# Kernel optimization log

Measured on AMD Instinct MI355X. Metric: run time of the kernel, lower is better.

Reference implementation:

```python
import jax, jax.numpy as jnp
import numpy as np

VOCAB = 32000
D = 512
OUT = 1000
L = 2
H = 8
HD = D // H
MAX_SEQ = 128
ALPHA = 0.5
B, S = 8, 128


def _layernorm(h, g, b, eps=1e-5):
    mu = jnp.mean(h, axis=-1, keepdims=True)
    var = jnp.mean(jnp.square(h - mu), axis=-1, keepdims=True)
    return (h - mu) * jax.lax.rsqrt(var + eps) * g + b


def setup_inputs() -> dict:
    key = jax.random.key(0)
    ks = jax.random.split(key, 20)
    sd = 1.0 / np.sqrt(D)
    inp = {
        "x": jax.random.randint(ks[0], (B, S), 0, VOCAB),
        "steps": 20,
        "tok_emb": jax.random.normal(ks[1], (VOCAB, D), jnp.float32) * 0.02,
        "pos_emb": jax.random.normal(ks[2], (MAX_SEQ, D), jnp.float32) * 0.02,
        # per-layer stacked weights (linear as x @ W + b)
        "Wq": jax.random.normal(ks[3], (L, D, D), jnp.float32) * sd,
        "bq": jnp.zeros((L, D), jnp.float32),
        "Wk": jax.random.normal(ks[4], (L, D, D), jnp.float32) * sd,
        "bk": jnp.zeros((L, D), jnp.float32),
        "Wv": jax.random.normal(ks[5], (L, D, D), jnp.float32) * sd,
        "bv": jnp.zeros((L, D), jnp.float32),
        "Wo": jax.random.normal(ks[6], (L, D, D), jnp.float32) * sd,
        "bo": jnp.zeros((L, D), jnp.float32),
        "W1": jax.random.normal(ks[7], (L, D, 2 * D), jnp.float32) * sd,
        "b1": jnp.zeros((L, 2 * D), jnp.float32),
        "W2": jax.random.normal(ks[8], (L, 2 * D, D), jnp.float32) * (1.0 / np.sqrt(2 * D)),
        "b2": jnp.zeros((L, D), jnp.float32),
        "ln1_g": jnp.ones((L, D), jnp.float32),
        "ln1_b": jnp.zeros((L, D), jnp.float32),
        "ln2_g": jnp.ones((L, D), jnp.float32),
        "ln2_b": jnp.zeros((L, D), jnp.float32),
        "head_w": jax.random.normal(ks[9], (D, OUT), jnp.float32) * sd,
        "head_b": jnp.zeros((OUT,), jnp.float32),
    }
    return inp


def _forward(x, steps, tok_emb, pos_emb, Wq, bq, Wk, bk, Wv, bv, Wo, bo,
             W1, b1, W2, b2, ln1_g, ln1_b, ln2_g, ln2_b, head_w, head_b):
    b, s = x.shape
    x_emb = tok_emb[x] + pos_emb[jnp.arange(s)][None, :, :]  # [B,S,D]
    scale = 1.0 / np.sqrt(HD)

    def step(h, _):
        for i in range(L):
            hn = _layernorm(h, ln1_g[i], ln1_b[i])
            q = (hn @ Wq[i] + bq[i]).reshape(b, s, H, HD)
            k = (hn @ Wk[i] + bk[i]).reshape(b, s, H, HD)
            v = (hn @ Wv[i] + bv[i]).reshape(b, s, H, HD)
            scores = jnp.einsum('bqhd,bkhd->bhqk', q, k) * scale
            attn = jax.nn.softmax(scores, axis=-1)
            o = jnp.einsum('bhqk,bkhd->bqhd', attn, v).reshape(b, s, D)
            h = h + (o @ Wo[i] + bo[i])
            hn2 = _layernorm(h, ln2_g[i], ln2_b[i])
            ffn = jax.nn.relu(hn2 @ W1[i] + b1[i]) @ W2[i] + b2[i]
            h_target = h + ffn + x_emb
            h = h + ALPHA * (jnp.tanh(h_target) - h)  # lerp(h, tanh(t), alpha)
        return h, None

    h0 = jnp.zeros_like(x_emb)
    h, _ = jax.lax.scan(step, h0, None, length=steps)
    return h.mean(axis=1) @ head_w + head_b  # [B, OUT]


def reference(x, steps, tok_emb, pos_emb, Wq, bq, Wk, bk, Wv, bv, Wo, bo,
              W1, b1, W2, b2, ln1_g, ln1_b, ln2_g, ln2_b, head_w, head_b):
    return _forward(x, steps, tok_emb, pos_emb, Wq, bq, Wk, bk, Wv, bv, Wo, bo,
                    W1, b1, W2, b2, ln1_g, ln1_b, ln2_g, ln2_b, head_w, head_b)
```

## Files before the change

kernel.cpp:

```cpp
#include <hip/hip_runtime.h>
#include <hip/hip_bf16.h>
#include <math.h>

#define NTOK 1024
#define DM   512
#define NB   256

typedef unsigned short u16;
typedef __attribute__((ext_vector_type(8))) short short8;
typedef __attribute__((ext_vector_type(4))) float f32x4;
typedef __attribute__((ext_vector_type(2))) float f32x2;
typedef __attribute__((address_space(1))) const void* as1cv;
typedef __attribute__((address_space(3))) void* as3v;

#define VM16 0x4F70
#define VM8  0x0F78
#define VM6  0x0F76
#define VM0  0x0F70

__device__ inline u16 f2bf(float f) {
  __hip_bfloat16 h = __float2bfloat16(f);
  return *reinterpret_cast<u16*>(&h);
}
__device__ inline float bf2f(u16 b) {
  union { unsigned u; float f; } x; x.u = (unsigned)b << 16; return x.f;
}
__device__ inline void split8(const float* v, short8& hi, short8& lo) {
#pragma unroll
  for (int j = 0; j < 8; j++) {
    u16 h = f2bf(v[j]);
    hi[j] = (short)h;
    lo[j] = (short)f2bf(v[j] - bf2f(h));
  }
}
__device__ __forceinline__ f32x4 MFMA(short8 a, short8 b, f32x4 c) {
  return __builtin_amdgcn_mfma_f32_16x16x32_bf16(a, b, c, 0, 0, 0);
}
__device__ __forceinline__ void atomAddF(float* p, float v) {
  __hip_atomic_fetch_add(p, v, __ATOMIC_RELAXED, __HIP_MEMORY_SCOPE_AGENT);
}

__device__ __forceinline__ f32x2 ldg_cs2(const float* p) {
  f32x2 r;
  asm volatile("global_load_dwordx2 %0, %1, off sc0 sc1" : "=v"(r) : "v"(p) : "memory");
  return r;
}
__device__ __forceinline__ void vmwait0() {
  asm volatile("s_waitcnt vmcnt(0)" ::: "memory");
  __builtin_amdgcn_sched_barrier(0);
}

enum { EP_RESID = 1, EP_TANHLERP = 3 };

struct KArgs {
  const int* x;
  const float* tok; const float* pos;
  const float* W[6];
  const float* bias6[6];
  const float* ln1g; const float* ln1b; const float* ln2g; const float* ln2b;
  const float* hw; const float* hb;
  float* out;
  float* xe; float* h;
  u16* obh; u16* obl;
  u16* ffh; u16* ffl;
  u16* vT;
  u16* Kg;
  float* hm;
  u16* WTh[6]; u16* WTl[6];
  float* ln1sum; float* ln2sum;
  unsigned* bar;
};

#define SMEM_BYTES 49152

__device__ __forceinline__ void bar_arrive(unsigned* ctr, int tid) {
  __syncthreads();
  if (tid == 0)
    __hip_atomic_fetch_add(ctr, 1u, __ATOMIC_RELEASE, __HIP_MEMORY_SCOPE_AGENT);
}
__device__ __forceinline__ void bar_wait(unsigned* ctr, unsigned target, int tid) {
  if (tid == 0) {
    while (__hip_atomic_load(ctr, __ATOMIC_RELAXED, __HIP_MEMORY_SCOPE_AGENT) < target)
      __builtin_amdgcn_s_sleep(2);
    __builtin_amdgcn_fence(__ATOMIC_ACQUIRE, "agent");
  }
  __syncthreads();
}
__device__ __forceinline__ void bar_arrive_fast(unsigned* myslot, unsigned ph, int tid) {
  asm volatile("s_waitcnt vmcnt(0) lgkmcnt(0)" ::: "memory");
  __syncthreads();
  if (tid == 0)
    __hip_atomic_store(myslot, ph, __ATOMIC_RELAXED, __HIP_MEMORY_SCOPE_AGENT);
}
__device__ __forceinline__ void bar_wait_fast(unsigned* slotbase, unsigned ph, int tid) {
  if (tid < 32) {
    while (__hip_atomic_load(slotbase + tid * 16, __ATOMIC_RELAXED,
                             __HIP_MEMORY_SCOPE_AGENT) < ph)
      __builtin_amdgcn_s_sleep(1);
  }
  __syncthreads();
  asm volatile("buffer_inv sc0" ::: "memory");
  asm volatile("s_waitcnt vmcnt(0)" ::: "memory");
}
__global__ void bar_init(unsigned* bar) {
  for (int i = threadIdx.x; i < 8192; i += 256) bar[i] = 0u;
}

__device__ __forceinline__ void dmaW64(const u16* gbase, int K, int k0, u16* lds, int tid) {
  const int wave = tid >> 6, lane = tid & 63;
#pragma unroll
  for (int i = 0; i < 2; i++) {
    const int lc = wave * 128 + i * 64 + lane;
    const int n = lc >> 3, sl = lc & 7;
    const int c = sl ^ (n & 7);
    const u16* g = gbase + (size_t)n * K + k0 + c * 8;
    u16* dst = lds + (size_t)(wave * 128 + i * 64) * 8;
    __builtin_amdgcn_global_load_lds((as1cv)(const void*)g, (as3v)(void*)dst, 16, 0, 0);
  }
}
__device__ __forceinline__ int boff64(int n, int cp) { return n * 64 + ((cp ^ (n & 7)) << 3); }

__device__ __forceinline__ void dmaW32(const u16* gbase, int K, int k0, u16* lds, int tid) {
  const int wave = tid >> 6, lane = tid & 63;
  const int lc = wave * 64 + lane;
  const int p = lc >> 3, s3 = lc & 7;
  const int c3 = s3 ^ (p & 7);
  const int n = p * 2 + (c3 >> 2);
  const int c = c3 & 3;
  const u16* g = gbase + (size_t)n * K + k0 + c * 8;
  u16* dst = lds + (size_t)(wave * 64) * 8;
  __builtin_amdgcn_global_load_lds((as1cv)(const void*)g, (as3v)(void*)dst, 16, 0, 0);
}
__device__ __forceinline__ int boff32(int n, int cq) {
  const int c3 = ((n & 1) << 2) | cq;
  return ((n >> 1) << 6) + ((c3 ^ ((n >> 1) & 7)) << 3);
}

__device__ __forceinline__ void pfBD2(const u16* bh0, const u16* bl0, int K, char* sm, int tid) {
  dmaW64(bh0, K, 0,  (u16*)sm, tid);
  dmaW64(bl0, K, 0,  (u16*)sm + 4096, tid);
  dmaW64(bh0, K, 64, (u16*)(sm + 16384), tid);
  dmaW64(bl0, K, 64, (u16*)(sm + 16384) + 4096, tid);
}
__device__ __forceinline__ void pfA(const KArgs& a, int l, int head, char* sm, int tid) {
  const size_t o = (size_t)l * 512 * 512 + (size_t)head * 64 * 512;
  const u16* wz[6] = { a.WTh[0] + o, a.WTl[0] + o, a.WTh[1] + o,
                       a.WTl[1] + o, a.WTh[2] + o, a.WTl[2] + o };
#pragma unroll
  for (int z = 0; z < 6; z++) dmaW32(wz[z], 512, 0, (u16*)sm + z * 2048, tid);
}

__device__ void phaseA1(const KArgs& a, int l, int head, int rbk, int grp,
                        const float* ln1, const float* hR,
                        u16* Kg_gh, u16* vT_gh, char* sm, int tid)
{
  const int wave = tid >> 6, lane = tid & 63;
  const int q = lane >> 4, r16 = lane & 15;
  const int wm = (wave >> 1) * 16, wn = (wave & 1) * 32;
  const int R0 = rbk * 32;
  const size_t wOff = (size_t)l * 512 * 512;
  const size_t hOff = (size_t)head * 64 * 512;

  const float* lg = a.ln1g + l * 512;
  const float* lb = a.ln1b + l * 512;
  const u16* wz[6] = { a.WTh[0] + wOff + hOff, a.WTl[0] + wOff + hOff,
                       a.WTh[1] + wOff + hOff, a.WTl[1] + wOff + hOff,
                       a.WTh[2] + wOff + hOff, a.WTl[2] + wOff + hOff };
  u16* buf[2] = { (u16*)sm, (u16*)sm + 12288 };

  f32x2 st = ldg_cs2(ln1 + (R0 + wm + r16) * 2);
  vmwait0();
  const float mu = st.x * (1.0f / 512.0f);
  const float iv = rsqrtf(st.y * (1.0f / 512.0f) - mu * mu + 1e-5f);

  f32x4 aq[2] = {}, ak[2] = {}, av[2] = {};
  float4 rA[2], rB4[2], rg[2], rb_[2], rg2[2], rb2[2];
  {
    const float* hp = hR + (size_t)(R0 + wm + r16) * DM + q * 8;
    rA[0] = *(const float4*)hp; rA[1] = *(const float4*)(hp + 4);
  }
  rg[0] = *(const float4*)&lg[q * 8]; rg[1] = *(const float4*)&lg[q * 8 + 4];
  rb_[0] = *(const float4*)&lb[q * 8]; rb_[1] = *(const float4*)&lb[q * 8 + 4];

  for (int ks = 0; ks < 16; ks++) {
    if (ks + 1 < 16) {
      const int kb = (ks + 1) * 32 + q * 8;
      const float* hp = hR + (size_t)(R0 + wm + r16) * DM + kb;
      rB4[0] = *(const float4*)hp; rB4[1] = *(const float4*)(hp + 4);
      rg2[0] = *(const float4*)&lg[kb]; rg2[1] = *(const float4*)&lg[kb + 4];
      rb2[0] = *(const float4*)&lb[kb]; rb2[1] = *(const float4*)&lb[kb + 4];
      __builtin_amdgcn_s_waitcnt(VM6);
    } else {
      __builtin_amdgcn_s_waitcnt(VM0);
    }
    __builtin_amdgcn_s_barrier();
    if (ks + 1 < 16) {
      u16* nb = buf[(ks + 1) & 1];
#pragma unroll
      for (int z2 = 0; z2 < 6; z2++) dmaW32(wz[z2], 512, (ks + 1) * 32, nb + z2 * 2048, tid);
    }
    const u16* cb = buf[ks & 1];
    short8 ah, al;
    {
      float v[8] = {
        (rA[0].x - mu) * iv * rg[0].x + rb_[0].x,
        (rA[0].y - mu) * iv * rg[0].y + rb_[0].y,
        (rA[0].z - mu) * iv * rg[0].z + rb_[0].z,
        (rA[0].w - mu) * iv * rg[0].w + rb_[0].w,
        (rA[1].x - mu) * iv * rg[1].x + rb_[1].x,
        (rA[1].y - mu) * iv * rg[1].y + rb_[1].y,
        (rA[1].z - mu) * iv * rg[1].z + rb_[1].z,
        (rA[1].w - mu) * iv * rg[1].w + rb_[1].w };
      split8(v, ah, al);
    }
#pragma unroll
    for (int z = 0; z < 3; z++) {
      f32x4* ac = (z == 0) ? aq : ((z == 1) ? ak : av);
#pragma unroll
      for (int fj = 0; fj < 2; fj++) {
        const int n = wn + fj * 16 + r16;
        const int off = boff32(n, q);
        short8 bh = *(const short8*)&cb[(z * 2) * 2048 + off];
        short8 bl = *(const short8*)&cb[(z * 2 + 1) * 2048 + off];
        ac[fj] = MFMA(ah, bh, ac[fj]);
        ac[fj] = MFMA(ah, bl, ac[fj]);
        ac[fj] = MFMA(al, bh, ac[fj]);
      }
    }
    rA[0] = rB4[0]; rA[1] = rB4[1];
    rg[0] = rg2[0]; rg[1] = rg2[1]; rb_[0] = rb2[0]; rb_[1] = rb2[1];
  }
  __syncthreads();

  u16 (*Qb)[66] = (u16(*)[66])sm;
  {
    const float* bq = a.bias6[0] + l * 512 + head * 64;
    const float* bk = a.bias6[1] + l * 512 + head * 64;
    const float* bv = a.bias6[2] + l * 512 + head * 64;
#pragma unroll
    for (int fj = 0; fj < 2; fj++) {
      const int col = wn + fj * 16 + r16;
      const int rl0 = wm + q * 4;
      const float bqv = bq[col], bkv = bk[col], bvv = bv[col];
#pragma unroll
      for (int i = 0; i < 4; i++) {
        Qb[rl0 + i][col] = f2bf(aq[fj][i] + bqv);
        Kg_gh[(size_t)(R0 + rl0 + i) * 64 + col] = f2bf(ak[fj][i] + bkv);
        vT_gh[(size_t)col * 128 + R0 + rl0 + i] = f2bf(av[fj][i] + bvv);
      }
    }
  }
}

__device__ void phaseA2(const KArgs& a, int head, int rbk,
                        const u16* Kg_gh, const u16* vT_gh,
                        u16* obh_g, u16* obl_g, char* sm, int tid)
{
  const int wave = tid >> 6, lane = tid & 63;
  const int q = lane >> 4, r16 = lane & 15;
  const int R0 = rbk * 32;
  u16 (*Qb)[66] = (u16(*)[66])sm;
  u16 (*Kb)[72] = (u16(*)[72])(sm + 4224);
  u16 (*Pb)[132] = (u16(*)[132])(sm + 22656);

#pragma unroll
  for (int c = 0; c < 4; c++) {
    const int lin = (c * 256 + tid) * 8;
    const int row = lin >> 6, col = lin & 63;
    *(short8*)&Kb[row][col] = *(const short8*)(Kg_gh + lin);
  }
  __syncthreads();

  f32x4 sc[8] = {};
  const int m0 = (wave & 1) * 16;
  if (wave < 2) {
#pragma unroll
    for (int kk = 0; kk < 2; kk++) {
      short8 aQ = *(const short8*)&Qb[m0 + r16][kk * 32 + q * 8];
#pragma unroll
      for (int nt = 0; nt < 8; nt++) {
        short8 bK = *(const short8*)&Kb[nt * 16 + r16][kk * 32 + q * 8];
        sc[nt] = MFMA(aQ, bK, sc[nt]);
      }
    }
#pragma unroll
    for (int i = 0; i < 4; i++) {
      float mrow = -1e30f;
#pragma unroll
      for (int nt = 0; nt < 8; nt++) {
        float v = sc[nt][i] * 0.125f; sc[nt][i] = v; mrow = fmaxf(mrow, v);
      }
#pragma unroll
      for (int o = 1; o < 16; o <<= 1) mrow = fmaxf(mrow, __shfl_xor(mrow, o, 64));
      float lsum = 0.f;
#pragma unroll
      for (int nt = 0; nt < 8; nt++) {
        float p = __expf(sc[nt][i] - mrow); sc[nt][i] = p; lsum += p;
      }
#pragma unroll
      for (int o = 1; o < 16; o <<= 1) lsum += __shfl_xor(lsum, o, 64);
      const float inv = 1.0f / lsum;
#pragma unroll
      for (int nt = 0; nt < 8; nt++) sc[nt][i] *= inv;
    }
#pragma unroll
    for (int nt = 0; nt < 8; nt++)
#pragma unroll
      for (int i = 0; i < 4; i++)
        Pb[m0 + q * 4 + i][nt * 16 + r16] = f2bf(sc[nt][i]);
  }
  __syncthreads();

  if (wave < 2) {
    f32x4 oa[4] = {};
#pragma unroll
    for (int kt = 0; kt < 4; kt++) {
      short8 aP = *(const short8*)&Pb[m0 + r16][kt * 32 + q * 8];
#pragma unroll
      for (int nt = 0; nt < 4; nt++) {
        short8 bV = *(const short8*)(vT_gh + (size_t)(nt * 16 + r16) * 128 + kt * 32 + q * 8);
        oa[nt] = MFMA(aP, bV, oa[nt]);
      }
    }
#pragma unroll
    for (int nt = 0; nt < 4; nt++)
#pragma unroll
      for (int i = 0; i < 4; i++) {
        const int row = R0 + m0 + q * 4 + i;
        const int col = head * 64 + nt * 16 + r16;
        float v = oa[nt][i];
        u16 hv = f2bf(v);
        obh_g[(size_t)row * DM + col] = hv;
        obl_g[(size_t)row * DM + col] = f2bf(v - bf2f(hv));
      }
  }
}

template<int EP>
__device__ void tileBD(const u16* Ahi, const u16* Alo, int K,
                       const u16* Whi, const u16* Wlo, const float* bias,
                       int bm, int bn, float* hIO, const float* Xx,
                       float* lnacc, char* sm, int tid)
{
  const int wave = tid >> 6, lane = tid & 63;
  const int q = lane >> 4, r16 = lane & 15;
  const int wm = (wave >> 1) * 16, wn = (wave & 1) * 32;
  const u16* bh0 = Whi + (size_t)bn * K;
  const u16* bl0 = Wlo + (size_t)bn * K;
  f32x4 acc[2] = {};
  const int nk = K >> 6;

  short8 cah[2], cal[2], nh[2], nl[2];
#pragma unroll
  for (int kk = 0; kk < 2; kk++) {
    const size_t ao = (size_t)(bm + wm + r16) * K + kk * 32 + q * 8;
    cah[kk] = *(const short8*)(Ahi + ao);
    cal[kk] = *(const short8*)(Alo + ao);
  }

  for (int ks = 0; ks < nk; ks++) {
    if (ks + 1 < nk) {
#pragma unroll
      for (int kk = 0; kk < 2; kk++) {
        const size_t ao = (size_t)(bm + wm + r16) * K + (ks + 1) * 64 + kk * 32 + q * 8;
        nh[kk] = *(const short8*)(Ahi + ao);
        nl[kk] = *(const short8*)(Alo + ao);
      }
      __builtin_amdgcn_s_waitcnt(VM8);
    } else {
      __builtin_amdgcn_s_waitcnt(VM0);
    }
    __builtin_amdgcn_s_barrier();
    if (ks + 2 < nk) {
      u16* slot = (u16*)(sm + ((ks + 2) % 3) * 16384);
      dmaW64(bh0, K, (ks + 2) * 64, slot, tid);
      dmaW64(bl0, K, (ks + 2) * 64, slot + 4096, tid);
    }
    const u16* Bsh = (const u16*)(sm + (ks % 3) * 16384);
    const u16* Bsl = Bsh + 4096;
#pragma unroll
    for (int kk = 0; kk < 2; kk++) {
#pragma unroll
      for (int fj = 0; fj < 2; fj++) {
        const int n = wn + fj * 16 + r16;
        const int off = boff64(n, kk * 4 + q);
        short8 bh = *(const short8*)&Bsh[off];
        short8 bl = *(const short8*)&Bsl[off];
        acc[fj] = MFMA(cah[kk], bh, acc[fj]);
        acc[fj] = MFMA(cah[kk], bl, acc[fj]);
        acc[fj] = MFMA(cal[kk], bh, acc[fj]);
      }
    }
#pragma unroll
    for (int kk = 0; kk < 2; kk++) { cah[kk] = nh[kk]; cal[kk] = nl[kk]; }
  }

  float outv[2][4];
#pragma unroll
  for (int fj = 0; fj < 2; fj++) {
    const int col = bn + wn + fj * 16 + r16;
    const float bvv = bias[col];
    const int row0 = bm + wm + q * 4;
#pragma unroll
    for (int i = 0; i < 4; i++) {
      const size_t off = (size_t)(row0 + i) * DM + col;
      if (EP == EP_RESID) {
        float hv = hIO[off] + acc[fj][i] + bvv;
        hIO[off] = hv; outv[fj][i] = hv;
      } else {
        float hv = hIO[off];
        float hn = 0.5f * hv + 0.5f * tanhf(hv + acc[fj][i] + bvv + Xx[off]);
        hIO[off] = hn; outv[fj][i] = hn;
      }
    }
  }
#pragma unroll
  for (int i = 0; i < 4; i++) {
    float a0 = outv[0][i], a1 = outv[1][i];
    float s1 = a0 + a1, s2 = a0 * a0 + a1 * a1;
#pragma unroll
    for (int o = 1; o < 16; o <<= 1) { s1 += __shfl_xor(s1, o, 64); s2 += __shfl_xor(s2, o, 64); }
    if (r16 == 0) {
      const int row = bm + wm + q * 4 + i;
      atomAddF(&lnacc[row * 2], s1);
      atomAddF(&lnacc[row * 2 + 1], s2);
    }
  }
}

__device__ void tileC2(const KArgs& a, int l, const float* h_g, const float* lnsrc,
                       u16* ffh_g, u16* ffl_g, int bm, int bn0, char* sm, int tid)
{
  const int wave = tid >> 6, lane = tid & 63;
  const int q = lane >> 4, r16 = lane & 15;
  const int wm = (wave >> 1) * 16, wn = (wave & 1) * 32;
  const size_t fOff = (size_t)l * 512 * 1024;
  const float* lg = a.ln2g + l * 512;
  const float* lb = a.ln2b + l * 512;

  f32x2 stl = ldg_cs2(lnsrc + (bm + wm + r16) * 2);
  vmwait0();
  const float mu = stl.x * (1.0f / 512.0f);
  const float iv = rsqrtf(stl.y * (1.0f / 512.0f) - mu * mu + 1e-5f);

  const u16* whB[2] = { a.WTh[4] + fOff + (size_t)bn0 * 512,
                        a.WTh[4] + fOff + (size_t)(bn0 + 512) * 512 };
  const u16* wlB[2] = { a.WTl[4] + fOff + (size_t)bn0 * 512,
                        a.WTl[4] + fOff + (size_t)(bn0 + 512) * 512 };
  const float* b1 = a.bias6[4] + l * 1024;
  f32x4 acc[2] = {};

  float4 rA[2][2], rB4[2][2], rg[2][2], rb[2][2], rg2[2][2], rb2[2][2];
#pragma unroll
  for (int kk = 0; kk < 2; kk++) {
    const int kb = kk * 32 + q * 8;
    const float* hp = h_g + (size_t)(bm + wm + r16) * DM + kb;
    rA[kk][0] = *(const float4*)hp; rA[kk][1] = *(const float4*)(hp + 4);
    rg[kk][0] = *(const float4*)&lg[kb]; rg[kk][1] = *(const float4*)&lg[kb + 4];
    rb[kk][0] = *(const float4*)&lb[kb]; rb[kk][1] = *(const float4*)&lb[kb + 4];
  }

  for (int s = 0; s < 16; s++) {
    if (s + 1 < 16) {
      const int kb1 = ((s + 1) & 7) * 64;
#pragma unroll
      for (int kk = 0; kk < 2; kk++) {
        const int kb = kb1 + kk * 32 + q * 8;
        const float* hp = h_g + (size_t)(bm + wm + r16) * DM + kb;
        rB4[kk][0] = *(const float4*)hp; rB4[kk][1] = *(const float4*)(hp + 4);
        rg2[kk][0] = *(const float4*)&lg[kb]; rg2[kk][1] = *(const float4*)&lg[kb + 4];
        rb2[kk][0] = *(const float4*)&lb[kb]; rb2[kk][1] = *(const float4*)&lb[kb + 4];
      }
      __builtin_amdgcn_s_waitcnt(VM16);
    } else {
      __builtin_amdgcn_s_waitcnt(VM0);
    }
    __builtin_amdgcn_s_barrier();
    if (s + 2 < 16) {
      const int t2 = (s + 2) >> 3, k2 = ((s + 2) & 7) * 64;
      u16* slot = (u16*)(sm + ((s + 2) % 3) * 16384);
      dmaW64(whB[t2], 512, k2, slot, tid);
      dmaW64(wlB[t2], 512, k2, slot + 4096, tid);
    }
    const u16* Bsh = (const u16*)(sm + (s % 3) * 16384);
    const u16* Bsl = Bsh + 4096;
#pragma unroll
    for (int kk = 0; kk < 2; kk++) {
      short8 ah, al;
      {
        float v[8] = {
          (rA[kk][0].x - mu) * iv * rg[kk][0].x + rb[kk][0].x,
          (rA[kk][0].y - mu) * iv * rg[kk][0].y + rb[kk][0].y,
          (rA[kk][0].z - mu) * iv * rg[kk][0].z + rb[kk][0].z,
          (rA[kk][0].w - mu) * iv * rg[kk][0].w + rb[kk][0].w,
          (rA[kk][1].x - mu) * iv * rg[kk][1].x + rb[kk][1].x,
          (rA[kk][1].y - mu) * iv * rg[kk][1].y + rb[kk][1].y,
          (rA[kk][1].z - mu) * iv * rg[kk][1].z + rb[kk][1].z,
          (rA[kk][1].w - mu) * iv * rg[kk][1].w + rb[kk][1].w };
        split8(v, ah, al);
      }
#pragma unroll
      for (int fj = 0; fj < 2; fj++) {
        const int n = wn + fj * 16 + r16;
        const int off = boff64(n, kk * 4 + q);
        short8 bh = *(const short8*)&Bsh[off];
        short8 bl = *(const short8*)&Bsl[off];
        acc[fj] = MFMA(ah, bh, acc[fj]);
        acc[fj] = MFMA(ah, bl, acc[fj]);
        acc[fj] = MFMA(al, bh, acc[fj]);
      }
    }
    if ((s & 7) == 7) {
      const int t = s >> 3;
#pragma unroll
      for (int fj = 0; fj < 2; fj++) {
        const int col = bn0 + t * 512 + wn + fj * 16 + r16;
        const float bvv = b1[col];
        const int row0 = bm + wm + q * 4;
#pragma unroll
        for (int i = 0; i < 4; i++) {
          const size_t off = (size_t)(row0 + i) * 1024 + col;
          float r = fmaxf(acc[fj][i] + bvv, 0.f);
          u16 hv = f2bf(r);
          ffh_g[off] = hv; ffl_g[off] = f2bf(r - bf2f(hv));
        }
        acc[fj] = (f32x4){0.f, 0.f, 0.f, 0.f};
      }
    }
#pragma unroll
    for (int kk = 0; kk < 2; kk++) {
      rA[kk][0] = rB4[kk][0]; rA[kk][1] = rB4[kk][1];
      rg[kk][0] = rg2[kk][0]; rg[kk][1] = rg2[kk][1];
      rb[kk][0] = rb2[kk][0]; rb[kk][1] = rb2[kk][1];
    }
  }
}

__global__ __launch_bounds__(256, 1) void persist(KArgs a)
{
  __shared__ __align__(16) char smem[SMEM_BYTES];
  const int tid = threadIdx.x;
  const int bid = blockIdx.x;

  unsigned myxcd;
  asm volatile("s_getreg_b32 %0, hwreg(HW_REG_XCC_ID)" : "=s"(myxcd));
  myxcd &= 15u;
  if (tid == 0) a.bar[512 + bid] = myxcd;

  {
    float (*tile)[33] = (float (*)[33])smem;
    const int tx = tid & 31, ty = tid >> 5;
    for (int t = bid; t < 4096; t += NB) {
      int tensor, z, k0, n0, K, N;
      if (t < 2048)      { tensor = t >> 9;  int rem = t & 511;  z = rem >> 8; int r2 = rem & 255;
                           K = 512;  N = 512;  k0 = (r2 >> 4) << 5; n0 = (r2 & 15) << 5; }
      else if (t < 3072) { tensor = 4;       int rem = t - 2048; z = rem >> 9; int r2 = rem & 511;
                           K = 512;  N = 1024; k0 = (r2 >> 5) << 5; n0 = (r2 & 31) << 5; }
      else               { tensor = 5;       int rem = t - 3072; z = rem >> 9; int r2 = rem & 511;
                           K = 1024; N = 512;  k0 = (r2 >> 4) << 5; n0 = (r2 & 15) << 5; }
      const float* src = a.W[tensor]   + (size_t)z * K * N;
      u16* dhi         = a.WTh[tensor] + (size_t)z * K * N;
      u16* dlo         = a.WTl[tensor] + (size_t)z * K * N;
      __syncthreads();
#pragma unroll
      for (int r = 0; r < 4; r++) {
        int k = ty + r * 8;
        tile[k][tx] = src[(size_t)(k0 + k) * N + n0 + tx];
      }
      __syncthreads();
#pragma unroll
      for (int r = 0; r < 4; r++) {
        int n = ty + r * 8;
        float w = tile[tx][n];
        u16 hi = f2bf(w);
        dhi[(size_t)(n0 + n) * K + k0 + tx] = hi;
        dlo[(size_t)(n0 + n) * K + k0 + tx] = f2bf(w - bf2f(hi));
      }
    }
    for (int idx = bid * 256 + tid; idx < NTOK * DM; idx += NB * 256) {
      int t = idx >> 9, d = idx & 511, ss = t & 127;
      a.xe[idx] = a.tok[(size_t)a.x[t] * DM + d] + a.pos[ss * DM + d];
      a.h[idx] = 0.0f;
    }
    const int nstat = (41 + 40) * 8 * 256;
    for (int idx = bid * 256 + tid; idx < nstat; idx += NB * 256)
      a.ln1sum[idx] = 0.0f;
  }
  bar_arrive(a.bar + 256, tid);
  bar_wait(a.bar + 256, NB, tid);

  int grp, gb; bool fast;
  {
    int cnt[8] = {0, 0, 0, 0, 0, 0, 0, 0};
    int rank = 0; bool bad = false;
    for (int j = 0; j < NB; j++) {
      unsigned xj = a.bar[512 + j];
      if (xj > 7u) { bad = true; }
      else {
        cnt[xj]++;
        if (xj == myxcd && j < bid) rank++;
      }
    }
    fast = !bad;
    for (int x2 = 0; x2 < 8; x2++) fast = fast && (cnt[x2] == 32);
    if (fast) { grp = (int)myxcd; gb = rank; }
    else      { grp = bid & 7;    gb = bid >> 3; }
  }

  const int head = gb & 7, rbk = gb >> 3;
  pfA(a, 0, head, smem, tid);

  unsigned* gctr = a.bar + grp * 32;
  unsigned* slotbase = a.bar + 1024 + grp * 512;
  unsigned* myslot = slotbase + gb * 16;
  unsigned tgt = 0, ph = 0;
  const size_t r512  = (size_t)grp * 128 * 512;
  const size_t r1024 = (size_t)grp * 128 * 1024;
  float* h_g  = a.h  + r512;
  float* xe_g = a.xe + r512;
  u16 *obh_g = a.obh + r512, *obl_g = a.obl + r512;
  u16 *ffh_g = a.ffh + r1024, *ffl_g = a.ffl + r1024;
  u16* Kg_gh = a.Kg + (size_t)(grp * 8 + head) * 128 * 64;
  u16* vT_gh = a.vT + (size_t)(grp * 8 + head) * 64 * 128;
  const int bn = (gb & 7) * 64, bm = (gb >> 3) * 32;

#define G_ARRIVE() do { ph++; if (fast) bar_arrive_fast(myslot, ph, tid); \
                        else bar_arrive(gctr, tid); } while (0)
#define G_WAIT()   do { if (fast) bar_wait_fast(slotbase, ph, tid); \
                        else { tgt += 32; bar_wait(gctr, tgt, tid); } } while (0)

  for (int it = 0; it < 40; it++) {
    const int l = it & 1;
    const size_t wOff = (size_t)l * 512 * 512;
    const size_t fOff = (size_t)l * 512 * 1024;
    float* ln1it = a.ln1sum + ((size_t)it * 8 + grp) * 256;
    float* ln2it = a.ln2sum + ((size_t)it * 8 + grp) * 256;
    float* ln1nx = a.ln1sum + ((size_t)(it + 1) * 8 + grp) * 256;

    phaseA1(a, l, head, rbk, grp, ln1it, h_g, Kg_gh, vT_gh, smem, tid);
    G_ARRIVE();
    G_WAIT();

    phaseA2(a, head, rbk, Kg_gh, vT_gh, obh_g, obl_g, smem, tid);
    G_ARRIVE();
    pfBD2(a.WTh[3] + wOff + (size_t)bn * 512, a.WTl[3] + wOff + (size_t)bn * 512, 512, smem, tid);
    G_WAIT();

    tileBD<EP_RESID>(obh_g, obl_g, 512, a.WTh[3] + wOff, a.WTl[3] + wOff,
                     a.bias6[3] + l * 512, bm, bn, h_g, nullptr, ln2it, smem, tid);
    G_ARRIVE();
    pfBD2(a.WTh[4] + fOff + (size_t)bn * 512, a.WTl[4] + fOff + (size_t)bn * 512, 512, smem, tid);
    G_WAIT();

    tileC2(a, l, h_g, ln2it, ffh_g, ffl_g, bm, bn, smem, tid);
    G_ARRIVE();
    pfBD2(a.WTh[5] + fOff + (size_t)bn * 1024, a.WTl[5] + fOff + (size_t)bn * 1024, 1024, smem, tid);
    G_WAIT();

    tileBD<EP_TANHLERP>(ffh_g, ffl_g, 1024, a.WTh[5] + fOff, a.WTl[5] + fOff,
                        a.bias6[5] + l * 512, bm, bn, h_g, xe_g, ln1nx, smem, tid);
    G_ARRIVE();
    if (it + 1 < 40) pfA(a, (it + 1) & 1, head, smem, tid);
    G_WAIT();
  }

  if (gb < 16) {
    const int dim = gb * 32 + (tid >> 3);
    const int sub = tid & 7;
    float sv = 0.f;
    for (int si = sub; si < 128; si += 8) sv += h_g[(size_t)si * DM + dim];
    sv += __shfl_xor(sv, 1, 64); sv += __shfl_xor(sv, 2, 64); sv += __shfl_xor(sv, 4, 64);
    if (sub == 0) a.hm[grp * 512 + dim] = sv * (1.0f / 128.0f);
  }
  G_ARRIVE();
  G_WAIT();

  {
    const int idx = tid >> 2;
    const int n = gb * 63 + idx;
    const int sub = tid & 3;
    if (idx < 63 && n < 1000) {
      const float* hr = a.hm + grp * 512 + sub * 128;
      const float* wr = a.hw + (size_t)(sub * 128) * 1000 + n;
      float sv = 0.f;
      for (int j = 0; j < 128; j++) sv = fmaf(hr[j], wr[(size_t)j * 1000], sv);
      sv += __shfl_xor(sv, 1, 64);
      sv += __shfl_xor(sv, 2, 64);
      if (sub == 0) a.out[grp * 1000 + n] = sv + a.hb[n];
    }
  }
#undef G_ARRIVE
#undef G_WAIT
}

extern "C" void kernel_launch(void* const* d_in, const int* in_sizes, int n_in,
                              void* d_out, int out_size, void* d_ws, size_t ws_size,
                              hipStream_t stream)
{
  (void)in_sizes; (void)n_in; (void)out_size; (void)ws_size;
  KArgs a;
  a.x    = (const int*)d_in[0];
  a.tok  = (const float*)d_in[2];
  a.pos  = (const float*)d_in[3];
  a.W[0] = (const float*)d_in[4];   a.bias6[0] = (const float*)d_in[5];
  a.W[1] = (const float*)d_in[6];   a.bias6[1] = (const float*)d_in[7];
  a.W[2] = (const float*)d_in[8];   a.bias6[2] = (const float*)d_in[9];
  a.W[3] = (const float*)d_in[10];  a.bias6[3] = (const float*)d_in[11];
  a.W[4] = (const float*)d_in[12];  a.bias6[4] = (const float*)d_in[13];
  a.W[5] = (const float*)d_in[14];  a.bias6[5] = (const float*)d_in[15];
  a.ln1g = (const float*)d_in[16];
  a.ln1b = (const float*)d_in[17];
  a.ln2g = (const float*)d_in[18];
  a.ln2b = (const float*)d_in[19];
  a.hw   = (const float*)d_in[20];
  a.hb   = (const float*)d_in[21];
  a.out  = (float*)d_out;

  char* ws = (char*)d_ws;
  const size_t MB = 1ull << 20;
  a.xe   = (float*)(ws + 0 * MB);
  a.h    = (float*)(ws + 2 * MB);
  a.obh  = (u16*)(ws + 4 * MB);
  a.obl  = (u16*)(ws + 5 * MB);
  a.ffh  = (u16*)(ws + 6 * MB);
  a.ffl  = (u16*)(ws + 8 * MB);
  a.hm   = (float*)(ws + 10 * MB);
  a.vT   = (u16*)(ws + 11 * MB);
  a.WTh[0] = (u16*)(ws + 12 * MB);  a.WTl[0] = (u16*)(ws + 13 * MB);
  a.WTh[1] = (u16*)(ws + 14 * MB);  a.WTl[1] = (u16*)(ws + 15 * MB);
  a.WTh[2] = (u16*)(ws + 16 * MB);  a.WTl[2] = (u16*)(ws + 17 * MB);
  a.WTh[3] = (u16*)(ws + 18 * MB);  a.WTl[3] = (u16*)(ws + 19 * MB);
  a.WTh[4] = (u16*)(ws + 20 * MB);  a.WTl[4] = (u16*)(ws + 22 * MB);
  a.WTh[5] = (u16*)(ws + 24 * MB);  a.WTl[5] = (u16*)(ws + 26 * MB);
  a.bar    = (unsigned*)(ws + 28 * MB);
  a.ln1sum = (float*)(ws + 29 * MB);
  a.ln2sum = a.ln1sum + (size_t)41 * 8 * 256;
  a.Kg     = (u16*)(ws + 30 * MB);

  bar_init<<<1, 256, 0, stream>>>(a.bar);
  persist<<<NB, 256, 0, stream>>>(a);
}
```

Before: 3.292 ms.

## Double persistent block count to 512 with 16-row tiles per block

```diff
diff --git a/kernel.cpp b/kernel.cpp
--- a/kernel.cpp
+++ b/kernel.cpp
@@ -4,7 +4,7 @@
 
 #define NTOK 1024
 #define DM   512
-#define NB   256
+#define NB   512
 
 typedef unsigned short u16;
 typedef __attribute__((ext_vector_type(8))) short short8;
@@ -93,7 +93,7 @@
     __hip_atomic_store(myslot, ph, __ATOMIC_RELAXED, __HIP_MEMORY_SCOPE_AGENT);
 }
 __device__ __forceinline__ void bar_wait_fast(unsigned* slotbase, unsigned ph, int tid) {
-  if (tid < 32) {
+  if (tid < 64) {
     while (__hip_atomic_load(slotbase + tid * 16, __ATOMIC_RELAXED,
                              __HIP_MEMORY_SCOPE_AGENT) < ph)
       __builtin_amdgcn_s_sleep(1);
@@ -103,7 +103,7 @@
   asm volatile("s_waitcnt vmcnt(0)" ::: "memory");
 }
 __global__ void bar_init(unsigned* bar) {
-  for (int i = threadIdx.x; i < 8192; i += 256) bar[i] = 0u;
+  for (int i = threadIdx.x; i < 16384; i += 256) bar[i] = 0u;
 }
 
 __device__ __forceinline__ void dmaW64(const u16* gbase, int K, int k0, u16* lds, int tid) {
@@ -156,8 +156,8 @@
 {
   const int wave = tid >> 6, lane = tid & 63;
   const int q = lane >> 4, r16 = lane & 15;
-  const int wm = (wave >> 1) * 16, wn = (wave & 1) * 32;
-  const int R0 = rbk * 32;
+  const int wn = wave * 16;
+  const int R0 = rbk * 16;
   const size_t wOff = (size_t)l * 512 * 512;
   const size_t hOff = (size_t)head * 64 * 512;
 
@@ -168,15 +168,15 @@
                        a.WTh[2] + wOff + hOff, a.WTl[2] + wOff + hOff };
   u16* buf[2] = { (u16*)sm, (u16*)sm + 12288 };
 
-  f32x2 st = ldg_cs2(ln1 + (R0 + wm + r16) * 2);
+  f32x2 st = ldg_cs2(ln1 + (R0 + r16) * 2);
   vmwait0();
   const float mu = st.x * (1.0f / 512.0f);
   const float iv = rsqrtf(st.y * (1.0f / 512.0f) - mu * mu + 1e-5f);
 
-  f32x4 aq[2] = {}, ak[2] = {}, av[2] = {};
+  f32x4 aq = {}, ak = {}, av = {};
   float4 rA[2], rB4[2], rg[2], rb_[2], rg2[2], rb2[2];
   {
-    const float* hp = hR + (size_t)(R0 + wm + r16) * DM + q * 8;
+    const float* hp = hR + (size_t)(R0 + r16) * DM + q * 8;
     rA[0] = *(const float4*)hp; rA[1] = *(const float4*)(hp + 4);
   }
   rg[0] = *(const float4*)&lg[q * 8]; rg[1] = *(const float4*)&lg[q * 8 + 4];
@@ -185,7 +185,7 @@
   for (int ks = 0; ks < 16; ks++) {
     if (ks + 1 < 16) {
       const int kb = (ks + 1) * 32 + q * 8;
-      const float* hp = hR + (size_t)(R0 + wm + r16) * DM + kb;
+      const float* hp = hR + (size_t)(R0 + r16) * DM + kb;
       rB4[0] = *(const float4*)hp; rB4[1] = *(const float4*)(hp + 4);
       rg2[0] = *(const float4*)&lg[kb]; rg2[1] = *(const float4*)&lg[kb + 4];
       rb2[0] = *(const float4*)&lb[kb]; rb2[1] = *(const float4*)&lb[kb + 4];
@@ -215,17 +215,14 @@
     }
 #pragma unroll
     for (int z = 0; z < 3; z++) {
-      f32x4* ac = (z == 0) ? aq : ((z == 1) ? ak : av);
-#pragma unroll
-      for (int fj = 0; fj < 2; fj++) {
-        const int n = wn + fj * 16 + r16;
-        const int off = boff32(n, q);
-        short8 bh = *(const short8*)&cb[(z * 2) * 2048 + off];
-        short8 bl = *(const short8*)&cb[(z * 2 + 1) * 2048 + off];
-        ac[fj] = MFMA(ah, bh, ac[fj]);
-        ac[fj] = MFMA(ah, bl, ac[fj]);
-        ac[fj] = MFMA(al, bh, ac[fj]);
-      }
+      f32x4* ac = (z == 0) ? &aq : ((z == 1) ? &ak : &av);
+      const int n = wn + r16;
+      const int off = boff32(n, q);
+      short8 bh = *(const short8*)&cb[(z * 2) * 2048 + off];
+      short8 bl = *(const short8*)&cb[(z * 2 + 1) * 2048 + off];
+      *ac = MFMA(ah, bh, *ac);
+      *ac = MFMA(ah, bl, *ac);
+      *ac = MFMA(al, bh, *ac);
     }
     rA[0] = rB4[0]; rA[1] = rB4[1];
     rg[0] = rg2[0]; rg[1] = rg2[1]; rb_[0] = rb2[0]; rb_[1] = rb2[1];
@@ -237,17 +234,14 @@
     const float* bq = a.bias6[0] + l * 512 + head * 64;
     const float* bk = a.bias6[1] + l * 512 + head * 64;
     const float* bv = a.bias6[2] + l * 512 + head * 64;
-#pragma unroll
-    for (int fj = 0; fj < 2; fj++) {
-      const int col = wn + fj * 16 + r16;
-      const int rl0 = wm + q * 4;
-      const float bqv = bq[col], bkv = bk[col], bvv = bv[col];
-#pragma unroll
-      for (int i = 0; i < 4; i++) {
-        Qb[rl0 + i][col] = f2bf(aq[fj][i] + bqv);
-        Kg_gh[(size_t)(R0 + rl0 + i) * 64 + col] = f2bf(ak[fj][i] + bkv);
-        vT_gh[(size_t)col * 128 + R0 + rl0 + i] = f2bf(av[fj][i] + bvv);
-      }
+    const int col = wn + r16;
+    const int rl0 = q * 4;
+    const float bqv = bq[col], bkv = bk[col], bvv = bv[col];
+#pragma unroll
+    for (int i = 0; i < 4; i++) {
+      Qb[rl0 + i][col] = f2bf(aq[i] + bqv);
+      Kg_gh[(size_t)(R0 + rl0 + i) * 64 + col] = f2bf(ak[i] + bkv);
+      vT_gh[(size_t)col * 128 + R0 + rl0 + i] = f2bf(av[i] + bvv);
     }
   }
 }
@@ -258,7 +252,7 @@
 {
   const int wave = tid >> 6, lane = tid & 63;
   const int q = lane >> 4, r16 = lane & 15;
-  const int R0 = rbk * 32;
+  const int R0 = rbk * 16;
   u16 (*Qb)[66] = (u16(*)[66])sm;
   u16 (*Kb)[72] = (u16(*)[72])(sm + 4224);
   u16 (*Pb)[132] = (u16(*)[132])(sm + 22656);
@@ -271,12 +265,11 @@
   }
   __syncthreads();
 
-  f32x4 sc[8] = {};
-  const int m0 = (wave & 1) * 16;
-  if (wave < 2) {
+  if (wave == 0) {
+    f32x4 sc[8] = {};
 #pragma unroll
     for (int kk = 0; kk < 2; kk++) {
-      short8 aQ = *(const short8*)&Qb[m0 + r16][kk * 32 + q * 8];
+      short8 aQ = *(const short8*)&Qb[r16][kk * 32 + q * 8];
 #pragma unroll
       for (int nt = 0; nt < 8; nt++) {
         short8 bK = *(const short8*)&Kb[nt * 16 + r16][kk * 32 + q * 8];
@@ -307,15 +300,15 @@
     for (int nt = 0; nt < 8; nt++)
 #pragma unroll
       for (int i = 0; i < 4; i++)
-        Pb[m0 + q * 4 + i][nt * 16 + r16] = f2bf(sc[nt][i]);
+        Pb[q * 4 + i][nt * 16 + r16] = f2bf(sc[nt][i]);
   }
   __syncthreads();
 
-  if (wave < 2) {
+  if (wave == 0) {
     f32x4 oa[4] = {};
 #pragma unroll
     for (int kt = 0; kt < 4; kt++) {
-      short8 aP = *(const short8*)&Pb[m0 + r16][kt * 32 + q * 8];
+      short8 aP = *(const short8*)&Pb[r16][kt * 32 + q * 8];
 #pragma unroll
       for (int nt = 0; nt < 4; nt++) {
         short8 bV = *(const short8*)(vT_gh + (size_t)(nt * 16 + r16) * 128 + kt * 32 + q * 8);
@@ -326,7 +319,7 @@
     for (int nt = 0; nt < 4; nt++)
 #pragma unroll
       for (int i = 0; i < 4; i++) {
-        const int row = R0 + m0 + q * 4 + i;
+        const int row = R0 + q * 4 + i;
         const int col = head * 64 + nt * 16 + r16;
         float v = oa[nt][i];
         u16 hv = f2bf(v);
@@ -344,16 +337,16 @@
 {
   const int wave = tid >> 6, lane = tid & 63;
   const int q = lane >> 4, r16 = lane & 15;
-  const int wm = (wave >> 1) * 16, wn = (wave & 1) * 32;
+  const int wn = wave * 16;
   const u16* bh0 = Whi + (size_t)bn * K;
   const u16* bl0 = Wlo + (size_t)bn * K;
-  f32x4 acc[2] = {};
+  f32x4 acc = {};
   const int nk = K >> 6;
 
   short8 cah[2], cal[2], nh[2], nl[2];
 #pragma unroll
   for (int kk = 0; kk < 2; kk++) {
-    const size_t ao = (size_t)(bm + wm + r16) * K + kk * 32 + q * 8;
+    const size_t ao = (size_t)(bm + r16) * K + kk * 32 + q * 8;
     cah[kk] = *(const short8*)(Ahi + ao);
     cal[kk] = *(const short8*)(Alo + ao);
   }
@@ -362,7 +355,7 @@
     if (ks + 1 < nk) {
 #pragma unroll
       for (int kk = 0; kk < 2; kk++) {
-        const size_t ao = (size_t)(bm + wm + r16) * K + (ks + 1) * 64 + kk * 32 + q * 8;
+        const size_t ao = (size_t)(bm + r16) * K + (ks + 1) * 64 + kk * 32 + q * 8;
         nh[kk] = *(const short8*)(Ahi + ao);
         nl[kk] = *(const short8*)(Alo + ao);
       }
@@ -380,48 +373,43 @@
     const u16* Bsl = Bsh + 4096;
 #pragma unroll
     for (int kk = 0; kk < 2; kk++) {
-#pragma unroll
-      for (int fj = 0; fj < 2; fj++) {
-        const int n = wn + fj * 16 + r16;
-        const int off = boff64(n, kk * 4 + q);
-        short8 bh = *(const short8*)&Bsh[off];
-        short8 bl = *(const short8*)&Bsl[off];
-        acc[fj] = MFMA(cah[kk], bh, acc[fj]);
-        acc[fj] = MFMA(cah[kk], bl, acc[fj]);
-        acc[fj] = MFMA(cal[kk], bh, acc[fj]);
-      }
+      const int n = wn + r16;
+      const int off = boff64(n, kk * 4 + q);
+      short8 bh = *(const short8*)&Bsh[off];
+      short8 bl = *(const short8*)&Bsl[off];
+      acc = MFMA(cah[kk], bh, acc);
+      acc = MFMA(cah[kk], bl, acc);
+      acc = MFMA(cal[kk], bh, acc);
     }
 #pragma unroll
     for (int kk = 0; kk < 2; kk++) { cah[kk] = nh[kk]; cal[kk] = nl[kk]; }
   }
 
-  float outv[2][4];
-#pragma unroll
-  for (int fj = 0; fj < 2; fj++) {
-    const int col = bn + wn + fj * 16 + r16;
+  float outv[4];
+  {
+    const int col = bn + wn + r16;
     const float bvv = bias[col];
-    const int row0 = bm + wm + q * 4;
+    const int row0 = bm + q * 4;
 #pragma unroll
     for (int i = 0; i < 4; i++) {
       const size_t off = (size_t)(row0 + i) * DM + col;
       if (EP == EP_RESID) {
-        float hv = hIO[off] + acc[fj][i] + bvv;
-        hIO[off] = hv; outv[fj][i] = hv;
+        float hv = hIO[off] + acc[i] + bvv;
+        hIO[off] = hv; outv[i] = hv;
       } else {
         float hv = hIO[off];
-        float hn = 0.5f * hv + 0.5f * tanhf(hv + acc[fj][i] + bvv + Xx[off]);
-        hIO[off] = hn; outv[fj][i] = hn;
+        float hn = 0.5f * hv + 0.5f * tanhf(hv + acc[i] + bvv + Xx[off]);
+        hIO[off] = hn; outv[i] = hn;
       }
     }
   }
 #pragma unroll
   for (int i = 0; i < 4; i++) {
-    float a0 = outv[0][i], a1 = outv[1][i];
-    float s1 = a0 + a1, s2 = a0 * a0 + a1 * a1;
+    float s1 = outv[i], s2 = outv[i] * outv[i];
 #pragma unroll
     for (int o = 1; o < 16; o <<= 1) { s1 += __shfl_xor(s1, o, 64); s2 += __shfl_xor(s2, o, 64); }
     if (r16 == 0) {
-      const int row = bm + wm + q * 4 + i;
+      const int row = bm + q * 4 + i;
       atomAddF(&lnacc[row * 2], s1);
       atomAddF(&lnacc[row * 2 + 1], s2);
     }
@@ -433,12 +421,12 @@
 {
   const int wave = tid >> 6, lane = tid & 63;
   const int q = lane >> 4, r16 = lane & 15;
-  const int wm = (wave >> 1) * 16, wn = (wave & 1) * 32;
+  const int wn = wave * 16;
   const size_t fOff = (size_t)l * 512 * 1024;
   const float* lg = a.ln2g + l * 512;
   const float* lb = a.ln2b + l * 512;
 
-  f32x2 stl = ldg_cs2(lnsrc + (bm + wm + r16) * 2);
+  f32x2 stl = ldg_cs2(lnsrc + (bm + r16) * 2);
   vmwait0();
   const float mu = stl.x * (1.0f / 512.0f);
   const float iv = rsqrtf(stl.y * (1.0f / 512.0f) - mu * mu + 1e-5f);
@@ -448,13 +436,13 @@
   const u16* wlB[2] = { a.WTl[4] + fOff + (size_t)bn0 * 512,
                         a.WTl[4] + fOff + (size_t)(bn0 + 512) * 512 };
   const float* b1 = a.bias6[4] + l * 1024;
-  f32x4 acc[2] = {};
+  f32x4 acc = {};
 
   float4 rA[2][2], rB4[2][2], rg[2][2], rb[2][2], rg2[2][2], rb2[2][2];
 #pragma unroll
   for (int kk = 0; kk < 2; kk++) {
     const int kb = kk * 32 + q * 8;
-    const float* hp = h_g + (size_t)(bm + wm + r16) * DM + kb;
+    const float* hp = h_g + (size_t)(bm + r16) * DM + kb;
     rA[kk][0] = *(const float4*)hp; rA[kk][1] = *(const float4*)(hp + 4);
     rg[kk][0] = *(const float4*)&lg[kb]; rg[kk][1] = *(const float4*)&lg[kb + 4];
     rb[kk][0] = *(const float4*)&lb[kb]; rb[kk][1] = *(const float4*)&lb[kb + 4];
@@ -466,7 +454,7 @@
 #pragma unroll
       for (int kk = 0; kk < 2; kk++) {
         const int kb = kb1 + kk * 32 + q * 8;
-        const float* hp = h_g + (size_t)(bm + wm + r16) * DM + kb;
+        const float* hp = h_g + (size_t)(bm + r16) * DM + kb;
         rB4[kk][0] = *(const float4*)hp; rB4[kk][1] = *(const float4*)(hp + 4);
         rg2[kk][0] = *(const float4*)&lg[kb]; rg2[kk][1] = *(const float4*)&lg[kb + 4];
         rb2[kk][0] = *(const float4*)&lb[kb]; rb2[kk][1] = *(const float4*)&lb[kb + 4];
@@ -499,33 +487,27 @@
           (rA[kk][1].w - mu) * iv * rg[kk][1].w + rb[kk][1].w };
         split8(v, ah, al);
       }
-#pragma unroll
-      for (int fj = 0; fj < 2; fj++) {
-        const int n = wn + fj * 16 + r16;
-        const int off = boff64(n, kk * 4 + q);
-        short8 bh = *(const short8*)&Bsh[off];
-        short8 bl = *(const short8*)&Bsl[off];
-        acc[fj] = MFMA(ah, bh, acc[fj]);
-        acc[fj] = MFMA(ah, bl, acc[fj]);
-        acc[fj] = MFMA(al, bh, acc[fj]);
-      }
+      const int n = wn + r16;
+      const int off = boff64(n, kk * 4 + q);
+      short8 bh = *(const short8*)&Bsh[off];
+      short8 bl = *(const short8*)&Bsl[off];
+      acc = MFMA(ah, bh, acc);
+      acc = MFMA(ah, bl, acc);
+      acc = MFMA(al, bh, acc);
     }
     if ((s & 7) == 7) {
       const int t = s >> 3;
-#pragma unroll
-      for (int fj = 0; fj < 2; fj++) {
-        const int col = bn0 + t * 512 + wn + fj * 16 + r16;
-        const float bvv = b1[col];
-        const int row0 = bm + wm + q * 4;
-#pragma unroll
-        for (int i = 0; i < 4; i++) {
-          const size_t off = (size_t)(row0 + i) * 1024 + col;
-          float r = fmaxf(acc[fj][i] + bvv, 0.f);
-          u16 hv = f2bf(r);
-          ffh_g[off] = hv; ffl_g[off] = f2bf(r - bf2f(hv));
-        }
-        acc[fj] = (f32x4){0.f, 0.f, 0.f, 0.f};
-      }
+      const int col = bn0 + t * 512 + wn + r16;
+      const float bvv = b1[col];
+      const int row0 = bm + q * 4;
+#pragma unroll
+      for (int i = 0; i < 4; i++) {
+        const size_t off = (size_t)(row0 + i) * 1024 + col;
+        float r = fmaxf(acc[i] + bvv, 0.f);
+        u16 hv = f2bf(r);
+        ffh_g[off] = hv; ffl_g[off] = f2bf(r - bf2f(hv));
+      }
+      acc = (f32x4){0.f, 0.f, 0.f, 0.f};
     }
 #pragma unroll
     for (int kk = 0; kk < 2; kk++) {
@@ -536,7 +518,7 @@
   }
 }
 
-__global__ __launch_bounds__(256, 1) void persist(KArgs a)
+__global__ __launch_bounds__(256, 2) void persist(KArgs a)
 {
   __shared__ __align__(16) char smem[SMEM_BYTES];
   const int tid = threadIdx.x;
@@ -602,7 +584,7 @@
       }
     }
     fast = !bad;
-    for (int x2 = 0; x2 < 8; x2++) fast = fast && (cnt[x2] == 32);
+    for (int x2 = 0; x2 < 8; x2++) fast = fast && (cnt[x2] == 64);
     if (fast) { grp = (int)myxcd; gb = rank; }
     else      { grp = bid & 7;    gb = bid >> 3; }
   }
@@ -611,7 +593,7 @@
   pfA(a, 0, head, smem, tid);
 
   unsigned* gctr = a.bar + grp * 32;
-  unsigned* slotbase = a.bar + 1024 + grp * 512;
+  unsigned* slotbase = a.bar + 1024 + grp * 1024;
   unsigned* myslot = slotbase + gb * 16;
   unsigned tgt = 0, ph = 0;
   const size_t r512  = (size_t)grp * 128 * 512;
@@ -622,12 +604,12 @@
   u16 *ffh_g = a.ffh + r1024, *ffl_g = a.ffl + r1024;
   u16* Kg_gh = a.Kg + (size_t)(grp * 8 + head) * 128 * 64;
   u16* vT_gh = a.vT + (size_t)(grp * 8 + head) * 64 * 128;
-  const int bn = (gb & 7) * 64, bm = (gb >> 3) * 32;
+  const int bn = (gb & 7) * 64, bm = (gb >> 3) * 16;
 
 #define G_ARRIVE() do { ph++; if (fast) bar_arrive_fast(myslot, ph, tid); \
                         else bar_arrive(gctr, tid); } while (0)
 #define G_WAIT()   do { if (fast) bar_wait_fast(slotbase, ph, tid); \
-                        else { tgt += 32; bar_wait(gctr, tgt, tid); } } while (0)
+                        else { tgt += 64; bar_wait(gctr, tgt, tid); } } while (0)
 
   for (int it = 0; it < 40; it++) {
     const int l = it & 1;
```

New measurement: 5.388 ms. 63.7% more time.
